# Kernel optimization log

Hardware: AMD Instinct MI355X
Metric: run time of the kernel (lower is better)

Reference implementation:

```python
import jax, jax.numpy as jnp
import numpy as np
from functools import partial

SUBSTEPS = 4  # fixed dopri5 substeps per output interval (adaptive control replaced by fixed grid)

# Dormand-Prince 5(4) tableau (5th-order solution row)
_C = (0.0, 1/5, 3/10, 4/5, 8/9, 1.0)
_A = (
    (),
    (1/5,),
    (3/40, 9/40),
    (44/45, -56/15, 32/9),
    (19372/6561, -25360/2187, 64448/6561, -212/729),
    (9017/3168, -355/33, 46732/5247, 49/176, -5103/18656),
)
_B = (35/384, 0.0, 500/1113, 125/192, -2187/6784, 11/84)


def _dopri5_step(f, y, t0, dt):
    ks = []
    for i in range(6):
        yi = y
        for aij, kj in zip(_A[i], ks):
            yi = yi + dt * aij * kj
        ks.append(f(t0 + _C[i] * dt, yi))
    y_new = y
    for bi, ki in zip(_B, ks):
        y_new = y_new + dt * bi * ki
    return y_new


def setup_inputs() -> dict:
    key = jax.random.key(0)
    k1, k2, k3 = jax.random.split(key, 3)
    B, D, H, T = 4096, 64, 256, 50
    y0 = jax.random.normal(k1, (B, D), dtype=jnp.float32)
    t = jnp.arange(T, dtype=jnp.float32) * 0.1
    W1 = jax.random.normal(k2, (D, H), dtype=jnp.float32) * (1.0 / np.sqrt(D))
    b1 = jnp.zeros((H,), dtype=jnp.float32)
    W2 = jax.random.normal(k3, (H, D), dtype=jnp.float32) * (1.0 / np.sqrt(H))
    b2 = jnp.zeros((D,), dtype=jnp.float32)
    return {"y0": y0, "t": t, "W1": W1, "b1": b1, "W2": W2, "b2": b2}


def reference(y0, t, W1, b1, W2, b2):
    # vector field: autonomous MLP (time arg kept for API fidelity)
    def f(ti, y):
        return jnp.tanh(y @ W1 + b1) @ W2 + b2

    def interval(y, tpair):
        t0, t1 = tpair
        dt = (t1 - t0) / SUBSTEPS
        def sub(yc, i):
            return _dopri5_step(f, yc, t0 + i * dt, dt), None
        y, _ = jax.lax.scan(sub, y, jnp.arange(SUBSTEPS, dtype=t.dtype))
        return y, y

    _, ys = jax.lax.scan(interval, y0, (t[:-1], t[1:]))
    # trajectory includes the initial state at t[0], like odeint
    return jnp.concatenate([y0[None], ys], axis=0)  # [T, B, D]
```

## Files before the change

kernel.cpp:

```cpp
#include <hip/hip_runtime.h>

#define NB 4096
#define ND 64
#define NH 256
#define NT 50
#define ROWS 8
#define THREADS 512
#define GRID (NB / ROWS)

#define YIS 84
#define ZS  324
#define RRS 68
#define RJS (8 * RRS)

__device__ __forceinline__ float fast_tanh(float x) {
  float e = __expf(2.0f * x);
  return 1.0f - 2.0f * __builtin_amdgcn_rcpf(e + 1.0f);
}

template <int CTRL>
__device__ __forceinline__ float dpp_add(float x) {
  int s = __builtin_amdgcn_update_dpp(0, __float_as_int(x), CTRL, 0xF, 0xF, true);
  return x + __int_as_float(s);
}
#define DPP_XOR1 0xB1
#define DPP_XOR2 0x4E

extern "C" __global__
__attribute__((amdgpu_flat_work_group_size(THREADS, THREADS)))
__attribute__((amdgpu_waves_per_eu(2, 4)))
void ode_kernel(const float* __restrict__ y0,
                const float* __restrict__ tt,
                const float* __restrict__ W1,
                const float* __restrict__ b1,
                const float* __restrict__ W2,
                const float* __restrict__ b2,
                float* __restrict__ out)
{
  __shared__ float sYI[ROWS * YIS];
  __shared__ float sZ [ROWS * ZS];
  __shared__ float sRed[4 * RJS];

  const int tid  = threadIdx.x;
  const int wv   = tid >> 6;
  const int lane = tid & 63;
  const int d    = lane;
  const int row  = (int)blockIdx.x * ROWS + wv;
  const int rh   = wv >> 2;
  const int q4   = lane & 3;
  const int jg   = (tid >> 2) & 63;
  const int jhi  = wv & 3;
  const int dg2  = lane >> 2;

  float w1_[16][4];
#pragma unroll
  for (int dd = 0; dd < 16; ++dd) {
    const float4 t = *(const float4*)&W1[(q4 * 16 + dd) * NH + 4 * jg];
    w1_[dd][0] = t.x; w1_[dd][1] = t.y; w1_[dd][2] = t.z; w1_[dd][3] = t.w;
  }
  const float4 b1v = *(const float4*)&b1[4 * jg];

  float w2_[16][4];
#pragma unroll
  for (int jj = 0; jj < 16; ++jj) {
    const float4 t = *(const float4*)&W2[((jhi * 4 + q4) * 16 + jj) * ND + 4 * dg2];
    w2_[jj][0] = t.x; w2_[jj][1] = t.y; w2_[jj][2] = t.z; w2_[jj][3] = t.w;
  }
  const float b2d = b2[d];

  float y = y0[row * ND + d];
  out[row * ND + d] = y;

  const int yi_woff = wv * YIS + (d >> 4) * 20 + (d & 15);
  const float* yib = &sYI[(rh * 4) * YIS + q4 * 20];
  float*       zwb = &sZ[(rh * 4) * ZS + (jg >> 2) * 20 + 4 * (jg & 3)];
  const float* zrb = &sZ[(rh * 4) * ZS + (jhi * 4 + q4) * 20];
  float*       rwb = &sRed[jhi * RJS + (rh * 4) * RRS + 4 * dg2];
  const float* rob = &sRed[wv * RRS + d];

  auto feval = [&](float yiv) -> float {
    sYI[yi_woff] = yiv;
    __syncthreads();

    float z[4][4];
#pragma unroll
    for (int r = 0; r < 4; ++r)
#pragma unroll
      for (int jj = 0; jj < 4; ++jj) z[r][jj] = 0.0f;
#pragma unroll
    for (int r = 0; r < 4; ++r) {
#pragma unroll
      for (int q = 0; q < 4; ++q) {
        const float4 a = *(const float4*)(yib + r * YIS + 4 * q);
#pragma unroll
        for (int jj = 0; jj < 4; ++jj) {
          z[r][jj] = fmaf(a.x, w1_[4 * q + 0][jj], z[r][jj]);
          z[r][jj] = fmaf(a.y, w1_[4 * q + 1][jj], z[r][jj]);
          z[r][jj] = fmaf(a.z, w1_[4 * q + 2][jj], z[r][jj]);
          z[r][jj] = fmaf(a.w, w1_[4 * q + 3][jj], z[r][jj]);
        }
      }
    }
#pragma unroll
    for (int r = 0; r < 4; ++r)
#pragma unroll
      for (int jj = 0; jj < 4; ++jj)
        z[r][jj] = dpp_add<DPP_XOR2>(dpp_add<DPP_XOR1>(z[r][jj]));
    if (q4 == 0) {
#pragma unroll
      for (int r = 0; r < 4; ++r) {
        float4 zv;
        zv.x = fast_tanh(z[r][0] + b1v.x);
        zv.y = fast_tanh(z[r][1] + b1v.y);
        zv.z = fast_tanh(z[r][2] + b1v.z);
        zv.w = fast_tanh(z[r][3] + b1v.w);
        *(float4*)(zwb + r * ZS) = zv;
      }
    }
    __syncthreads();

    float p[4][4];
#pragma unroll
    for (int r = 0; r < 4; ++r)
#pragma unroll
      for (int dd = 0; dd < 4; ++dd) p[r][dd] = 0.0f;
#pragma unroll
    for (int r = 0; r < 4; ++r) {
#pragma unroll
      for (int q = 0; q < 4; ++q) {
        const float4 a = *(const float4*)(zrb + r * ZS + 4 * q);
#pragma unroll
        for (int dd = 0; dd < 4; ++dd) {
          p[r][dd] = fmaf(a.x, w2_[4 * q + 0][dd], p[r][dd]);
          p[r][dd] = fmaf(a.y, w2_[4 * q + 1][dd], p[r][dd]);
          p[r][dd] = fmaf(a.z, w2_[4 * q + 2][dd], p[r][dd]);
          p[r][dd] = fmaf(a.w, w2_[4 * q + 3][dd], p[r][dd]);
        }
      }
    }
#pragma unroll
    for (int r = 0; r < 4; ++r)
#pragma unroll
      for (int dd = 0; dd < 4; ++dd)
        p[r][dd] = dpp_add<DPP_XOR2>(dpp_add<DPP_XOR1>(p[r][dd]));
    if (q4 == 0) {
#pragma unroll
      for (int r = 0; r < 4; ++r)
        *(float4*)(rwb + r * RRS) = make_float4(p[r][0], p[r][1], p[r][2], p[r][3]);
    }
    __syncthreads();

    float o = b2d;
#pragma unroll
    for (int jh = 0; jh < 4; ++jh) o += rob[jh * RJS];
    return o;
  };

  const float A10 = (float)(1.0 / 5.0);
  const float A20 = (float)(3.0 / 40.0),      A21 = (float)(9.0 / 40.0);
  const float A30 = (float)(44.0 / 45.0),     A31 = (float)(-56.0 / 15.0),
              A32 = (float)(32.0 / 9.0);
  const float A40 = (float)(19372.0 / 6561.0), A41 = (float)(-25360.0 / 2187.0),
              A42 = (float)(64448.0 / 6561.0), A43 = (float)(-212.0 / 729.0);
  const float A50 = (float)(9017.0 / 3168.0),  A51 = (float)(-355.0 / 33.0),
              A52 = (float)(46732.0 / 5247.0), A53 = (float)(49.0 / 176.0),
              A54 = (float)(-5103.0 / 18656.0);
  const float B0 = (float)(35.0 / 384.0),      B2 = (float)(500.0 / 1113.0),
              B3 = (float)(125.0 / 192.0),     B4 = (float)(-2187.0 / 6784.0),
              B5 = (float)(11.0 / 84.0);

  for (int ti = 0; ti < NT - 1; ++ti) {
    const float dt = (tt[ti + 1] - tt[ti]) * 0.25f;
    for (int ss = 0; ss < 4; ++ss) {
      const float k0 = feval(y);

      float yi = fmaf(dt * A10, k0, y);
      const float k1 = feval(yi);

      yi = y;
      yi = fmaf(dt * A20, k0, yi); yi = fmaf(dt * A21, k1, yi);
      const float k2 = feval(yi);

      yi = y;
      yi = fmaf(dt * A30, k0, yi); yi = fmaf(dt * A31, k1, yi);
      yi = fmaf(dt * A32, k2, yi);
      const float k3 = feval(yi);

      yi = y;
      yi = fmaf(dt * A40, k0, yi); yi = fmaf(dt * A41, k1, yi);
      yi = fmaf(dt * A42, k2, yi); yi = fmaf(dt * A43, k3, yi);
      const float k4 = feval(yi);

      yi = y;
      yi = fmaf(dt * A50, k0, yi); yi = fmaf(dt * A51, k1, yi);
      yi = fmaf(dt * A52, k2, yi); yi = fmaf(dt * A53, k3, yi);
      yi = fmaf(dt * A54, k4, yi);
      const float k5 = feval(yi);

      y = fmaf(dt * B0, k0, y);
      y = fmaf(dt * B2, k2, y);
      y = fmaf(dt * B3, k3, y);
      y = fmaf(dt * B4, k4, y);
      y = fmaf(dt * B5, k5, y);
    }
    out[(size_t)(ti + 1) * NB * ND + row * ND + d] = y;
  }
}

extern "C" void kernel_launch(void* const* d_in, const int* in_sizes, int n_in,
                              void* d_out, int out_size, void* d_ws, size_t ws_size,
                              hipStream_t stream) {
  const float* y0 = (const float*)d_in[0];
  const float* tt = (const float*)d_in[1];
  const float* W1 = (const float*)d_in[2];
  const float* b1 = (const float*)d_in[3];
  const float* W2 = (const float*)d_in[4];
  const float* b2 = (const float*)d_in[5];
  float* out = (float*)d_out;

  hipLaunchKernelGGL(ode_kernel, dim3(GRID), dim3(THREADS), 0, stream,
                     y0, tt, W1, b1, W2, b2, out);
}
```

Measured before the change: 5.709 ms.

## Use packed FP32 FMA with 8-row by 2-column thread tiles and asm DPP adds

Changes the per-thread work split from 4 rows by 4 columns to 8 rows by 2 columns, so each thread holds W1/W2 slices as float2 pairs. This lets both matmuls use v_pk_fma_f32, which does two FMAs per instruction with the activation broadcast through op_sel. The quad reductions become single inline-asm v_add_f32_dpp instructions instead of separate update_dpp plus add. The aim is fewer VALU issue slots per feval. The cost is more LDS reads per thread, since all 8 rows are loaded instead of 4, and inline asm that limits compiler scheduling.

```diff
diff --git a/kernel.cpp b/kernel.cpp
--- a/kernel.cpp
+++ b/kernel.cpp
@@ -11,20 +11,40 @@
 #define YIS 84
 #define ZS  324
 #define RRS 68
-#define RJS (8 * RRS)
+#define RJS (ROWS * RRS)
+
+typedef float f2 __attribute__((ext_vector_type(2)));
+typedef float f4 __attribute__((ext_vector_type(4)));
 
 __device__ __forceinline__ float fast_tanh(float x) {
   float e = __expf(2.0f * x);
   return 1.0f - 2.0f * __builtin_amdgcn_rcpf(e + 1.0f);
 }
 
-template <int CTRL>
-__device__ __forceinline__ float dpp_add(float x) {
-  int s = __builtin_amdgcn_update_dpp(0, __float_as_int(x), CTRL, 0xF, 0xF, true);
-  return x + __int_as_float(s);
-}
-#define DPP_XOR1 0xB1
-#define DPP_XOR2 0x4E
+__device__ __forceinline__ float dpp_add_x1(float x) {
+  float d;
+  asm("v_add_f32_dpp %0, %1, %1 quad_perm:[1,0,3,2] row_mask:0xf bank_mask:0xf"
+      : "=v"(d) : "v"(x));
+  return d;
+}
+__device__ __forceinline__ float dpp_add_x2(float x) {
+  float d;
+  asm("v_add_f32_dpp %0, %1, %1 quad_perm:[2,3,0,1] row_mask:0xf bank_mask:0xf"
+      : "=v"(d) : "v"(x));
+  return d;
+}
+__device__ __forceinline__ float quad_reduce(float x) {
+  return dpp_add_x2(dpp_add_x1(x));
+}
+
+__device__ __forceinline__ void pk_fma_lo(f2 a, f2 b, f2& c) {
+  asm("v_pk_fma_f32 %0, %1, %2, %0 op_sel:[0,0,0] op_sel_hi:[0,1,1]"
+      : "+v"(c) : "v"(a), "v"(b));
+}
+__device__ __forceinline__ void pk_fma_hi(f2 a, f2 b, f2& c) {
+  asm("v_pk_fma_f32 %0, %1, %2, %0 op_sel:[1,0,0] op_sel_hi:[1,1,1]"
+      : "+v"(c) : "v"(a), "v"(b));
+}
 
 extern "C" __global__
 __attribute__((amdgpu_flat_work_group_size(THREADS, THREADS)))
@@ -46,107 +66,94 @@
   const int lane = tid & 63;
   const int d    = lane;
   const int row  = (int)blockIdx.x * ROWS + wv;
-  const int rh   = wv >> 2;
   const int q4   = lane & 3;
-  const int jg   = (tid >> 2) & 63;
-  const int jhi  = wv & 3;
-  const int dg2  = lane >> 2;
-
-  float w1_[16][4];
-#pragma unroll
-  for (int dd = 0; dd < 16; ++dd) {
-    const float4 t = *(const float4*)&W1[(q4 * 16 + dd) * NH + 4 * jg];
-    w1_[dd][0] = t.x; w1_[dd][1] = t.y; w1_[dd][2] = t.z; w1_[dd][3] = t.w;
-  }
-  const float4 b1v = *(const float4*)&b1[4 * jg];
-
-  float w2_[16][4];
-#pragma unroll
-  for (int jj = 0; jj < 16; ++jj) {
-    const float4 t = *(const float4*)&W2[((jhi * 4 + q4) * 16 + jj) * ND + 4 * dg2];
-    w2_[jj][0] = t.x; w2_[jj][1] = t.y; w2_[jj][2] = t.z; w2_[jj][3] = t.w;
-  }
+  const int jp   = tid >> 2;
+  const int jc   = (wv & 3) * 4 + q4;
+  const int dp   = (lane >> 2) | ((wv >> 2) << 4);
+
+  f2 w1p[16];
+#pragma unroll
+  for (int dd = 0; dd < 16; ++dd)
+    w1p[dd] = *(const f2*)&W1[(q4 * 16 + dd) * NH + 2 * jp];
+  const f2 b1p = *(const f2*)&b1[2 * jp];
+
+  f2 w2p[16];
+#pragma unroll
+  for (int jj = 0; jj < 16; ++jj)
+    w2p[jj] = *(const f2*)&W2[(jc * 16 + jj) * ND + 2 * dp];
   const float b2d = b2[d];
 
   float y = y0[row * ND + d];
   out[row * ND + d] = y;
 
   const int yi_woff = wv * YIS + (d >> 4) * 20 + (d & 15);
-  const float* yib = &sYI[(rh * 4) * YIS + q4 * 20];
-  float*       zwb = &sZ[(rh * 4) * ZS + (jg >> 2) * 20 + 4 * (jg & 3)];
-  const float* zrb = &sZ[(rh * 4) * ZS + (jhi * 4 + q4) * 20];
-  float*       rwb = &sRed[jhi * RJS + (rh * 4) * RRS + 4 * dg2];
+  const float* yib = &sYI[q4 * 20];
+  float*       zwb = &sZ[(jp >> 3) * 20 + ((2 * jp) & 15)];
+  const float* zrb = &sZ[jc * 20];
+  float*       rwb = &sRed[(wv & 3) * RJS + 2 * dp];
   const float* rob = &sRed[wv * RRS + d];
 
   auto feval = [&](float yiv) -> float {
     sYI[yi_woff] = yiv;
     __syncthreads();
 
-    float z[4][4];
-#pragma unroll
-    for (int r = 0; r < 4; ++r)
-#pragma unroll
-      for (int jj = 0; jj < 4; ++jj) z[r][jj] = 0.0f;
-#pragma unroll
-    for (int r = 0; r < 4; ++r) {
+    f2 z2[8];
+#pragma unroll
+    for (int r = 0; r < 8; ++r) z2[r] = (f2)0.0f;
+#pragma unroll
+    for (int r = 0; r < 8; ++r) {
 #pragma unroll
       for (int q = 0; q < 4; ++q) {
-        const float4 a = *(const float4*)(yib + r * YIS + 4 * q);
-#pragma unroll
-        for (int jj = 0; jj < 4; ++jj) {
-          z[r][jj] = fmaf(a.x, w1_[4 * q + 0][jj], z[r][jj]);
-          z[r][jj] = fmaf(a.y, w1_[4 * q + 1][jj], z[r][jj]);
-          z[r][jj] = fmaf(a.z, w1_[4 * q + 2][jj], z[r][jj]);
-          z[r][jj] = fmaf(a.w, w1_[4 * q + 3][jj], z[r][jj]);
-        }
+        const f4 a = *(const f4*)(yib + r * YIS + 4 * q);
+        const f2 a01 = __builtin_shufflevector(a, a, 0, 1);
+        const f2 a23 = __builtin_shufflevector(a, a, 2, 3);
+        pk_fma_lo(a01, w1p[4 * q + 0], z2[r]);
+        pk_fma_hi(a01, w1p[4 * q + 1], z2[r]);
+        pk_fma_lo(a23, w1p[4 * q + 2], z2[r]);
+        pk_fma_hi(a23, w1p[4 * q + 3], z2[r]);
       }
     }
 #pragma unroll
-    for (int r = 0; r < 4; ++r)
-#pragma unroll
-      for (int jj = 0; jj < 4; ++jj)
-        z[r][jj] = dpp_add<DPP_XOR2>(dpp_add<DPP_XOR1>(z[r][jj]));
+    for (int r = 0; r < 8; ++r) {
+      z2[r].x = quad_reduce(z2[r].x);
+      z2[r].y = quad_reduce(z2[r].y);
+    }
     if (q4 == 0) {
 #pragma unroll
-      for (int r = 0; r < 4; ++r) {
-        float4 zv;
-        zv.x = fast_tanh(z[r][0] + b1v.x);
-        zv.y = fast_tanh(z[r][1] + b1v.y);
-        zv.z = fast_tanh(z[r][2] + b1v.z);
-        zv.w = fast_tanh(z[r][3] + b1v.w);
-        *(float4*)(zwb + r * ZS) = zv;
+      for (int r = 0; r < 8; ++r) {
+        f2 zv;
+        zv.x = fast_tanh(z2[r].x + b1p.x);
+        zv.y = fast_tanh(z2[r].y + b1p.y);
+        *(f2*)(zwb + r * ZS) = zv;
       }
     }
     __syncthreads();
 
-    float p[4][4];
-#pragma unroll
-    for (int r = 0; r < 4; ++r)
-#pragma unroll
-      for (int dd = 0; dd < 4; ++dd) p[r][dd] = 0.0f;
-#pragma unroll
-    for (int r = 0; r < 4; ++r) {
+    f2 p2[8];
+#pragma unroll
+    for (int r = 0; r < 8; ++r) p2[r] = (f2)0.0f;
+#pragma unroll
+    for (int r = 0; r < 8; ++r) {
 #pragma unroll
       for (int q = 0; q < 4; ++q) {
-        const float4 a = *(const float4*)(zrb + r * ZS + 4 * q);
-#pragma unroll
-        for (int dd = 0; dd < 4; ++dd) {
-          p[r][dd] = fmaf(a.x, w2_[4 * q + 0][dd], p[r][dd]);
-          p[r][dd] = fmaf(a.y, w2_[4 * q + 1][dd], p[r][dd]);
-          p[r][dd] = fmaf(a.z, w2_[4 * q + 2][dd], p[r][dd]);
-          p[r][dd] = fmaf(a.w, w2_[4 * q + 3][dd], p[r][dd]);
-        }
+        const f4 a = *(const f4*)(zrb + r * ZS + 4 * q);
+        const f2 a01 = __builtin_shufflevector(a, a, 0, 1);
+        const f2 a23 = __builtin_shufflevector(a, a, 2, 3);
+        pk_fma_lo(a01, w2p[4 * q + 0], p2[r]);
+        pk_fma_hi(a01, w2p[4 * q + 1], p2[r]);
+        pk_fma_lo(a23, w2p[4 * q + 2], p2[r]);
+        pk_fma_hi(a23, w2p[4 * q + 3], p2[r]);
       }
     }
 #pragma unroll
-    for (int r = 0; r < 4; ++r)
-#pragma unroll
-      for (int dd = 0; dd < 4; ++dd)
-        p[r][dd] = dpp_add<DPP_XOR2>(dpp_add<DPP_XOR1>(p[r][dd]));
+    for (int r = 0; r < 8; ++r) {
+      p2[r].x = quad_reduce(p2[r].x);
+      p2[r].y = quad_reduce(p2[r].y);
+    }
     if (q4 == 0) {
 #pragma unroll
-      for (int r = 0; r < 4; ++r)
-        *(float4*)(rwb + r * RRS) = make_float4(p[r][0], p[r][1], p[r][2], p[r][3]);
+      for (int r = 0; r < 8; ++r)
+        *(f2*)(rwb + r * RRS) = p2[r];
     }
     __syncthreads();
 
```

Measured after the change: 5.163 ms (median of 2 runs). 9.6% less time.
